# Performance work log

Measured on AMD Instinct MI355X. Metric: run time of the kernel, lower is better.

Reference implementation:

```python
import jax, jax.numpy as jnp
import numpy as np

B, LA, LB = 16, 2048, 2048
DA, DB, DH = 768, 512, 512
EPS = 1e-5


def _layer_norm(x, g, b):
    mu = jnp.mean(x, axis=-1, keepdims=True)
    var = jnp.var(x, axis=-1, keepdims=True)
    return (x - mu) * jax.lax.rsqrt(var + EPS) * g + b


def setup_inputs() -> dict:
    key = jax.random.key(0)
    ks = jax.random.split(key, 12)
    s = lambda d: 1.0 / np.sqrt(d)
    return {
        "z_a": jax.random.normal(ks[0], (B, LA, DA), jnp.float32),
        "z_b": jax.random.normal(ks[1], (B, LB, DB), jnp.float32),
        "Wa": jax.random.uniform(ks[2], (DA, DH), jnp.float32, -s(DA), s(DA)),
        "ba": jnp.zeros((DH,), jnp.float32),
        "Wb": jax.random.uniform(ks[3], (DB, DH), jnp.float32, -s(DB), s(DB)),
        "bb": jnp.zeros((DH,), jnp.float32),
        "W_co": jax.random.normal(ks[4], (DH, DH), jnp.float32),
        "Woa": jax.random.uniform(ks[5], (DH, DA), jnp.float32, -s(DH), s(DH)),
        "boa": jnp.zeros((DA,), jnp.float32),
        "Wob": jax.random.uniform(ks[6], (DH, DB), jnp.float32, -s(DH), s(DH)),
        "bob": jnp.zeros((DB,), jnp.float32),
        "ga": jnp.ones((DA,), jnp.float32),
        "beta_a": jnp.zeros((DA,), jnp.float32),
        "gb": jnp.ones((DB,), jnp.float32),
        "beta_b": jnp.zeros((DB,), jnp.float32),
    }


def reference(z_a, z_b, Wa, ba, Wb, bb, W_co, Woa, boa, Wob, bob, ga, beta_a, gb, beta_b):
    # projections to shared hidden space
    h_a = jnp.einsum('bld,dh->blh', z_a, Wa) + ba          # (B, LA, DH)
    h_b = jnp.einsum('bld,dh->blh', z_b, Wb) + bb          # (B, LB, DH)
    # bilinear tanh co-attention scores
    C = jnp.tanh(jnp.einsum('bih,hk,bjk->bij', h_a, W_co, h_b))  # (B, LA, LB)
    attn_a = jax.nn.softmax(C, axis=-1)                    # rows: over LB
    attn_b = jax.nn.softmax(C.transpose(0, 2, 1), axis=-1) # cols: over LA
    h_a_co = jnp.einsum('bij,bjh->bih', attn_a, h_b)       # (B, LA, DH)
    h_b_co = jnp.einsum('bji,bih->bjh', attn_b, h_a)       # (B, LB, DH)
    z_a_co = jnp.einsum('blh,hd->bld', h_a_co, Woa) + boa
    z_b_co = jnp.einsum('blh,hd->bld', h_b_co, Wob) + bob
    z_a_out = _layer_norm(z_a + z_a_co, ga, beta_a)
    z_b_out = _layer_norm(z_b + z_b_co, gb, beta_b)
    return (z_a_out, z_b_out)
```

## Files before the change

### kernel.cpp

```cpp
#include <hip/hip_runtime.h>
#include <stdint.h>

typedef short bf16x8 __attribute__((ext_vector_type(8)));
typedef float f32x4 __attribute__((ext_vector_type(4)));

#define BM 256
#define BN 128
#define BK 64
#define ABUF_U 16384
#define BUF_U  24576

#define AS1 __attribute__((address_space(1)))
#define AS3 __attribute__((address_space(3)))

__device__ __forceinline__ ushort f2bf(float x) {
    uint32_t u = __float_as_uint(x);
    u += 0x7FFFu + ((u >> 16) & 1u);
    return (ushort)(u >> 16);
}

__device__ __forceinline__ void gload16(const void* g, void* l) {
    __builtin_amdgcn_global_load_lds((const AS1 void*)g, (AS3 void*)l, 16, 0, 0);
}

template<int MODE, bool HAS_BIAS, bool WRITE_T>
__global__ __launch_bounds__(512)
void gemm_bt(const ushort* __restrict__ Aptr_, const ushort* __restrict__ Bptr_,
             void* __restrict__ Cptr_, ushort* __restrict__ CTptr_,
             const float* __restrict__ bias, const float* __restrict__ resid_,
             float* __restrict__ rsum_, float* __restrict__ csum_,
             const float* __restrict__ scale_,
             int M, int N, int K, int lda, int ldb, int ldc,
             long sA, long sB, long sC, long sCT, long sSum,
             int ldct, int rbshift)
{
    extern __shared__ ushort smem[];

    const int z    = blockIdx.z;
    const int m0   = blockIdx.x * BM;
    const int n0   = blockIdx.y * BN;
    const int tid  = threadIdx.x;
    const int lane = tid & 63;
    const int wave = tid >> 6;
    const int wr   = wave >> 2;
    const int wcn  = wave & 3;
    const int g    = lane >> 4, c = lane & 15;

    const ushort* Ap = Aptr_ + z * sA;
    const ushort* Bp = Bptr_ + z * sB;

    long aoff[4]; int aLds[4];
    #pragma unroll
    for (int u = 0; u < 4; ++u) {
        const int li  = u * 512 + tid;
        const int row = li >> 3;
        const int gck = (li & 7) ^ (row & 7);
        aoff[u] = (long)(m0 + row) * lda + gck * 8;
        aLds[u] = li * 8;
    }
    long boff[2]; int bLds[2];
    #pragma unroll
    for (int v = 0; v < 2; ++v) {
        const int li  = v * 512 + tid;
        const int row = li >> 3;
        const int gck = (li & 7) ^ (row & 7);
        boff[v] = (long)(n0 + row) * ldb + gck * 8;
        bLds[v] = li * 8;
    }

    auto stage3 = [&](int kt, ushort* As, ushort* Bs, int q) {
        if (q == 0) {
            gload16(Ap + aoff[0] + kt, As + aLds[0]);
            gload16(Ap + aoff[1] + kt, As + aLds[1]);
            gload16(Ap + aoff[2] + kt, As + aLds[2]);
        } else {
            gload16(Ap + aoff[3] + kt, As + aLds[3]);
            gload16(Bp + boff[0] + kt, Bs + bLds[0]);
            gload16(Bp + boff[1] + kt, Bs + bLds[1]);
        }
    };

    f32x4 acc[8][2] = {};

    const int nk = K / BK;
    stage3(0, smem, smem + ABUF_U, 0);
    stage3(0, smem, smem + ABUF_U, 1);
    stage3(BK, smem + BUF_U, smem + BUF_U + ABUF_U, 0);
    stage3(BK, smem + BUF_U, smem + BUF_U + ABUF_U, 1);
    asm volatile("s_waitcnt vmcnt(6)" ::: "memory");
    __builtin_amdgcn_s_barrier();

    int bt = 0;
    for (int t = 0; t < nk; ++t) {
        const int b2 = (bt + 2 >= 3) ? bt - 1 : bt + 2;
        ushort* As  = smem + bt * BUF_U;
        ushort* Bs  = As + ABUF_U;
        ushort* As2 = smem + b2 * BUF_U;
        ushort* Bs2 = As2 + ABUF_U;
        const bool pf = (t + 2 < nk);

        #pragma unroll
        for (int q = 0; q < 2; ++q) {
            bf16x8 af[8], bfr[2];
            #pragma unroll
            for (int mi = 0; mi < 8; ++mi) {
                const int row = wr * 128 + mi * 16 + c;
                const int ckq = (q * 4 + g) ^ (row & 7);
                af[mi] = *(const bf16x8*)&As[row * BK + ckq * 8];
            }
            #pragma unroll
            for (int ni = 0; ni < 2; ++ni) {
                const int row = wcn * 32 + ni * 16 + c;
                const int ckq = (q * 4 + g) ^ (row & 7);
                bfr[ni] = *(const bf16x8*)&Bs[row * BK + ckq * 8];
            }
            if (pf) stage3((t + 2) * BK, As2, Bs2, q);
            if (q == 1) {
                if (pf) asm volatile("s_waitcnt vmcnt(6)" ::: "memory");
                else    asm volatile("s_waitcnt vmcnt(0)" ::: "memory");
            }
            asm volatile("" ::: "memory");
            __builtin_amdgcn_s_barrier();
            __builtin_amdgcn_s_setprio(1);
            #pragma unroll
            for (int mi = 0; mi < 8; ++mi)
                #pragma unroll
                for (int ni = 0; ni < 2; ++ni)
                    acc[mi][ni] = __builtin_amdgcn_mfma_f32_16x16x32_bf16(af[mi], bfr[ni], acc[mi][ni], 0, 0, 0);
            __builtin_amdgcn_s_setprio(0);
            asm volatile("" ::: "memory");
            __builtin_amdgcn_s_barrier();
        }
        bt = (bt + 1 == 3) ? 0 : bt + 1;
    }

    if constexpr (MODE == 0) {
        ushort* Cp = (ushort*)Cptr_ + z * sC;
        #pragma unroll
        for (int mi = 0; mi < 8; ++mi) {
            const int row = m0 + wr * 128 + mi * 16 + g * 4;
            #pragma unroll
            for (int ni = 0; ni < 2; ++ni) {
                const int col = n0 + wcn * 32 + ni * 16 + c;
                const float bv = HAS_BIAS ? bias[col] : 0.f;
                ushort v[4];
                #pragma unroll
                for (int r = 0; r < 4; ++r) v[r] = f2bf(acc[mi][ni][r] + bv);
                #pragma unroll
                for (int r = 0; r < 4; ++r) Cp[(long)(row + r) * ldc + col] = v[r];
                if constexpr (WRITE_T) {
                    const int bb = row >> rbshift;
                    const int ii = row & ((1 << rbshift) - 1);
                    *(ushort4*)&CTptr_[(long)bb * sCT + (long)col * ldct + ii] =
                        make_ushort4(v[0], v[1], v[2], v[3]);
                }
            }
        }
    } else if constexpr (MODE == 1) {
        ushort* Ep  = (ushort*)Cptr_ + z * sC;
        ushort* ETp = CTptr_ + z * sCT;
        float* rs = rsum_ + z * sSum;
        float* cs = csum_ + z * sSum;
        float rowpart[8][4] = {};
        float colpart[2] = {};
        #pragma unroll
        for (int mi = 0; mi < 8; ++mi) {
            const int row = m0 + wr * 128 + mi * 16 + g * 4;
            #pragma unroll
            for (int ni = 0; ni < 2; ++ni) {
                const int col = n0 + wcn * 32 + ni * 16 + c;
                ushort v[4];
                #pragma unroll
                for (int r = 0; r < 4; ++r) {
                    const float s = acc[mi][ni][r];
                    const float t = 1.f - 2.f / (__expf(2.f * s) + 1.f);
                    const float e = __expf(t);
                    rowpart[mi][r] += e;
                    colpart[ni]    += e;
                    v[r] = f2bf(e);
                }
                #pragma unroll
                for (int r = 0; r < 4; ++r) Ep[(long)(row + r) * ldc + col] = v[r];
                *(ushort4*)&ETp[(long)col * ldct + row] = make_ushort4(v[0], v[1], v[2], v[3]);
            }
        }
        #pragma unroll
        for (int mi = 0; mi < 8; ++mi) {
            #pragma unroll
            for (int r = 0; r < 4; ++r) {
                float v = rowpart[mi][r];
                v += __shfl_xor(v, 1); v += __shfl_xor(v, 2);
                v += __shfl_xor(v, 4); v += __shfl_xor(v, 8);
                if (c == 0) atomicAdd(&rs[m0 + wr * 128 + mi * 16 + g * 4 + r], v);
            }
        }
        #pragma unroll
        for (int ni = 0; ni < 2; ++ni) {
            float v = colpart[ni];
            v += __shfl_xor(v, 16); v += __shfl_xor(v, 32);
            if (g == 0) atomicAdd(&cs[n0 + wcn * 32 + ni * 16 + c], v);
        }
    } else if constexpr (MODE == 2) {
        const float* sc = scale_ + z * sSum;
        ushort* Cp = (ushort*)Cptr_ + z * sC;
        #pragma unroll
        for (int mi = 0; mi < 8; ++mi) {
            const int row = m0 + wr * 128 + mi * 16 + g * 4;
            float rcp[4];
            #pragma unroll
            for (int r = 0; r < 4; ++r) rcp[r] = 1.f / sc[row + r];
            #pragma unroll
            for (int ni = 0; ni < 2; ++ni) {
                const int col = n0 + wcn * 32 + ni * 16 + c;
                #pragma unroll
                for (int r = 0; r < 4; ++r)
                    Cp[(long)(row + r) * ldc + col] = f2bf(acc[mi][ni][r] * rcp[r]);
            }
        }
    } else {
        float* Co = (float*)Cptr_;
        #pragma unroll
        for (int mi = 0; mi < 8; ++mi) {
            const int row = m0 + wr * 128 + mi * 16 + g * 4;
            #pragma unroll
            for (int ni = 0; ni < 2; ++ni) {
                const int col = n0 + wcn * 32 + ni * 16 + c;
                const float bv = bias[col];
                #pragma unroll
                for (int r = 0; r < 4; ++r) {
                    const long idx = (long)(row + r) * ldc + col;
                    Co[idx] = acc[mi][ni][r] + bv + resid_[idx];
                }
            }
        }
    }
}

__global__ __launch_bounds__(256)
void cast32to16(const float* __restrict__ in, ushort* __restrict__ out, long n) {
    const long stride = (long)gridDim.x * 256 * 8;
    for (long i = ((long)blockIdx.x * 256 + threadIdx.x) * 8; i < n; i += stride) {
        const float4 f0 = *(const float4*)(in + i);
        const float4 f1 = *(const float4*)(in + i + 4);
        uint4 w;
        w.x = (uint)f2bf(f0.x) | ((uint)f2bf(f0.y) << 16);
        w.y = (uint)f2bf(f0.z) | ((uint)f2bf(f0.w) << 16);
        w.z = (uint)f2bf(f1.x) | ((uint)f2bf(f1.y) << 16);
        w.w = (uint)f2bf(f1.z) | ((uint)f2bf(f1.w) << 16);
        *(uint4*)(out + i) = w;
    }
}

__global__ __launch_bounds__(256)
void tcast(const float* __restrict__ in, ushort* __restrict__ out, int R, int C) {
    __shared__ float t[32][33];
    const int bx = blockIdx.x * 32, by = blockIdx.y * 32;
    const int tx = threadIdx.x, ty = threadIdx.y;
    for (int i = ty; i < 32; i += 8) {
        const int r = by + i, cc = bx + tx;
        if (r < R && cc < C) t[i][tx] = in[(long)r * C + cc];
    }
    __syncthreads();
    for (int i = ty; i < 32; i += 8) {
        const int cc = bx + i, r = by + tx;
        if (cc < C && r < R) out[(long)cc * R + r] = f2bf(t[tx][i]);
    }
}

template<int D>
__global__ __launch_bounds__(256)
void ln_rows(float* __restrict__ y, const float* __restrict__ gam, const float* __restrict__ bet) {
    constexpr int NV = D / 256;
    const long row = blockIdx.x;
    float* p = y + row * D;
    const int tid = threadIdx.x;
    float v[NV];
    float s = 0.f, s2 = 0.f;
    #pragma unroll
    for (int k = 0; k < NV; ++k) {
        v[k] = p[tid + k * 256];
        s += v[k]; s2 += v[k] * v[k];
    }
    #pragma unroll
    for (int off = 1; off < 64; off <<= 1) {
        s  += __shfl_xor(s, off);
        s2 += __shfl_xor(s2, off);
    }
    __shared__ float ws[4], ws2[4];
    const int wave = tid >> 6, lane = tid & 63;
    if (lane == 0) { ws[wave] = s; ws2[wave] = s2; }
    __syncthreads();
    s  = ws[0] + ws[1] + ws[2] + ws[3];
    s2 = ws2[0] + ws2[1] + ws2[2] + ws2[3];
    const float mu  = s / D;
    const float var = s2 / D - mu * mu;
    const float rstd = rsqrtf(var + 1e-5f);
    #pragma unroll
    for (int k = 0; k < NV; ++k) {
        const int i = tid + k * 256;
        p[i] = (v[k] - mu) * rstd * gam[i] + bet[i];
    }
}

extern "C" void kernel_launch(void* const* d_in, const int* in_sizes, int n_in,
                              void* d_out, int out_size, void* d_ws, size_t ws_size,
                              hipStream_t stream)
{
    (void)in_sizes; (void)n_in; (void)out_size; (void)ws_size;
    const float* z_a    = (const float*)d_in[0];
    const float* z_b    = (const float*)d_in[1];
    const float* Wa     = (const float*)d_in[2];
    const float* ba     = (const float*)d_in[3];
    const float* Wb     = (const float*)d_in[4];
    const float* bb     = (const float*)d_in[5];
    const float* Wco    = (const float*)d_in[6];
    const float* Woa    = (const float*)d_in[7];
    const float* boa    = (const float*)d_in[8];
    const float* Wob    = (const float*)d_in[9];
    const float* bob    = (const float*)d_in[10];
    const float* ga     = (const float*)d_in[11];
    const float* beta_a = (const float*)d_in[12];
    const float* gb     = (const float*)d_in[13];
    const float* beta_b = (const float*)d_in[14];

    const int Bn = 16, LA = 2048, LB = 2048, DA = 768, DB = 512, DH = 512;
    const long MA = (long)Bn * LA;
    const long MB = (long)Bn * LB;

    char* w = (char*)d_ws;
    size_t off = 0;
    auto alc = [&](size_t bytes) { void* p = w + off; off += (bytes + 255) & ~(size_t)255; return p; };

    ushort* WaT  = (ushort*)alc((size_t)DH * DA * 2);
    ushort* WbT  = (ushort*)alc((size_t)DH * DB * 2);
    ushort* WcoT = (ushort*)alc((size_t)DH * DH * 2);
    ushort* WoaT = (ushort*)alc((size_t)DA * DH * 2);
    ushort* WobT = (ushort*)alc((size_t)DB * DH * 2);
    ushort* h_a  = (ushort*)alc((size_t)MA * DH * 2);
    ushort* h_b  = (ushort*)alc((size_t)MB * DH * 2);
    ushort* h_aT = (ushort*)alc((size_t)Bn * DH * LA * 2);
    ushort* h_bT = (ushort*)alc((size_t)Bn * DH * LB * 2);
    ushort* Ma   = (ushort*)alc((size_t)MA * DH * 2);
    ushort* E    = (ushort*)alc((size_t)Bn * LA * LB * 2);
    ushort* ET   = (ushort*)alc((size_t)Bn * LB * LA * 2);
    ushort* Pa   = (ushort*)alc((size_t)MA * DH * 2);
    ushort* Pb   = (ushort*)alc((size_t)MB * DH * 2);
    float*  rsum = (float*)alc((size_t)Bn * LA * 4);
    float*  csum = (float*)alc((size_t)Bn * LB * 4);

    ushort* za16 = E;
    ushort* zb16 = E + (size_t)MA * DA;

    dim3 blk(512, 1, 1);
    dim3 blk256(256, 1, 1);
    dim3 tb(32, 8, 1);
    const int SHM = 3 * BUF_U * 2;

    tcast<<<dim3(DH / 32, DA / 32, 1), tb, 0, stream>>>(Wa,  WaT,  DA, DH);
    tcast<<<dim3(DH / 32, DB / 32, 1), tb, 0, stream>>>(Wb,  WbT,  DB, DH);
    tcast<<<dim3(DH / 32, DH / 32, 1), tb, 0, stream>>>(Wco, WcoT, DH, DH);
    tcast<<<dim3(DA / 32, DH / 32, 1), tb, 0, stream>>>(Woa, WoaT, DH, DA);
    tcast<<<dim3(DB / 32, DH / 32, 1), tb, 0, stream>>>(Wob, WobT, DH, DB);

    cast32to16<<<dim3(2048, 1, 1), blk256, 0, stream>>>(z_a, za16, MA * DA);
    cast32to16<<<dim3(2048, 1, 1), blk256, 0, stream>>>(z_b, zb16, MB * DB);

    hipMemsetAsync(rsum, 0, (size_t)Bn * (LA + LB) * sizeof(float), stream);

    gemm_bt<0, true, true><<<dim3(MA / BM, DH / BN, 1), blk, SHM, stream>>>(
        za16, WaT, h_a, h_aT, ba, nullptr, nullptr, nullptr, nullptr,
        (int)MA, DH, DA, DA, DA, DH, 0, 0, 0, (long)DH * LA, 0, LA, 11);

    gemm_bt<0, true, true><<<dim3(MB / BM, DH / BN, 1), blk, SHM, stream>>>(
        zb16, WbT, h_b, h_bT, bb, nullptr, nullptr, nullptr, nullptr,
        (int)MB, DH, DB, DB, DB, DH, 0, 0, 0, (long)DH * LB, 0, LB, 11);

    gemm_bt<0, false, false><<<dim3(MA / BM, DH / BN, 1), blk, SHM, stream>>>(
        h_a, WcoT, Ma, nullptr, nullptr, nullptr, nullptr, nullptr, nullptr,
        (int)MA, DH, DH, DH, DH, DH, 0, 0, 0, 0, 0, 0, 0);

    gemm_bt<1, false, false><<<dim3(LA / BM, LB / BN, Bn), blk, SHM, stream>>>(
        Ma, h_b, E, ET, nullptr, nullptr, rsum, csum, nullptr,
        LA, LB, DH, DH, DH, LB,
        (long)LA * DH, (long)LB * DH, (long)LA * LB, (long)LB * LA, LA, LA, 0);

    gemm_bt<2, false, false><<<dim3(LA / BM, DH / BN, Bn), blk, SHM, stream>>>(
        E, h_bT, Pa, nullptr, nullptr, nullptr, nullptr, nullptr, rsum,
        LA, DH, LB, LB, LB, DH,
        (long)LA * LB, (long)DH * LB, (long)LA * DH, 0, LA, 0, 0);

    gemm_bt<2, false, false><<<dim3(LB / BM, DH / BN, Bn), blk, SHM, stream>>>(
        ET, h_aT, Pb, nullptr, nullptr, nullptr, nullptr, nullptr, csum,
        LB, DH, LA, LA, LA, DH,
        (long)LB * LA, (long)DH * LA, (long)LB * DH, 0, LB, 0, 0);

    float* outA = (float*)d_out;
    float* outB = outA + MA * DA;

    gemm_bt<3, true, false><<<dim3(MA / BM, DA / BN, 1), blk, SHM, stream>>>(
        Pa, WoaT, outA, nullptr, boa, z_a, nullptr, nullptr, nullptr,
        (int)MA, DA, DH, DH, DH, DA, 0, 0, 0, 0, 0, 0, 0);

    gemm_bt<3, true, false><<<dim3(MB / BM, DB / BN, 1), blk, SHM, stream>>>(
        Pb, WobT, outB, nullptr, bob, z_b, nullptr, nullptr, nullptr,
        (int)MB, DB, DH, DH, DH, DB, 0, 0, 0, 0, 0, 0, 0);

    ln_rows<768><<<dim3((unsigned)MA, 1, 1), blk256, 0, stream>>>(outA, ga, beta_a);
    ln_rows<512><<<dim3((unsigned)MB, 1, 1), blk256, 0, stream>>>(outB, gb, beta_b);
}
```

Measured before the change: 781.6 us.

## Widen GEMM tile to 256x256 with double-buffered, interleaved load/MFMA schedule

```diff
diff --git a/kernel.cpp b/kernel.cpp
--- a/kernel.cpp
+++ b/kernel.cpp
@@ -5,10 +5,10 @@
 typedef float f32x4 __attribute__((ext_vector_type(4)));
 
 #define BM 256
-#define BN 128
+#define BN 256
 #define BK 64
 #define ABUF_U 16384
-#define BUF_U  24576
+#define BUF_U  32768
 
 #define AS1 __attribute__((address_space(1)))
 #define AS3 __attribute__((address_space(3)))
@@ -23,8 +23,14 @@
     __builtin_amdgcn_global_load_lds((const AS1 void*)g, (AS3 void*)l, 16, 0, 0);
 }
 
+#define ISSUE2(kt, buf, i0)                                                          \
+    do {                                                                             \
+        gload16(((i0) < 4 ? Ap : Bp) + goff[i0] + (kt), smem + (buf)*BUF_U + loff[i0]); \
+        gload16((((i0)+1) < 4 ? Ap : Bp) + goff[(i0)+1] + (kt), smem + (buf)*BUF_U + loff[(i0)+1]); \
+    } while (0)
+
 template<int MODE, bool HAS_BIAS, bool WRITE_T>
-__global__ __launch_bounds__(512)
+__global__ __launch_bounds__(512, 2)
 void gemm_bt(const ushort* __restrict__ Aptr_, const ushort* __restrict__ Bptr_,
              void* __restrict__ Cptr_, ushort* __restrict__ CTptr_,
              const float* __restrict__ bias, const float* __restrict__ resid_,
@@ -49,89 +55,94 @@
     const ushort* Ap = Aptr_ + z * sA;
     const ushort* Bp = Bptr_ + z * sB;
 
-    long aoff[4]; int aLds[4];
+    long goff[8]; int loff[8];
     #pragma unroll
     for (int u = 0; u < 4; ++u) {
         const int li  = u * 512 + tid;
         const int row = li >> 3;
         const int gck = (li & 7) ^ (row & 7);
-        aoff[u] = (long)(m0 + row) * lda + gck * 8;
-        aLds[u] = li * 8;
-    }
-    long boff[2]; int bLds[2];
-    #pragma unroll
-    for (int v = 0; v < 2; ++v) {
-        const int li  = v * 512 + tid;
-        const int row = li >> 3;
-        const int gck = (li & 7) ^ (row & 7);
-        boff[v] = (long)(n0 + row) * ldb + gck * 8;
-        bLds[v] = li * 8;
-    }
-
-    auto stage3 = [&](int kt, ushort* As, ushort* Bs, int q) {
-        if (q == 0) {
-            gload16(Ap + aoff[0] + kt, As + aLds[0]);
-            gload16(Ap + aoff[1] + kt, As + aLds[1]);
-            gload16(Ap + aoff[2] + kt, As + aLds[2]);
+        goff[u]     = (long)(m0 + row) * lda + gck * 8;
+        loff[u]     = li * 8;
+        goff[u + 4] = (long)(n0 + row) * ldb + gck * 8;
+        loff[u + 4] = ABUF_U + li * 8;
+    }
+
+    f32x4 acc[8][4] = {};
+
+    const int nk = K / BK;
+    ISSUE2(0, 0, 0); ISSUE2(0, 0, 2); ISSUE2(0, 0, 4); ISSUE2(0, 0, 6);
+
+    for (int t = 0; t < nk; ++t) {
+        const int cur = t & 1, nxt = cur ^ 1;
+        const ushort* As = smem + cur * BUF_U;
+        const ushort* Bs = As + ABUF_U;
+        const bool pf = (t + 1 < nk);
+        const int kt1 = (t + 1) * BK;
+
+        if (pf) {
+            ISSUE2(kt1, nxt, 0);
+            asm volatile("s_waitcnt vmcnt(2)" ::: "memory");
         } else {
-            gload16(Ap + aoff[3] + kt, As + aLds[3]);
-            gload16(Bp + boff[0] + kt, Bs + bLds[0]);
-            gload16(Bp + boff[1] + kt, Bs + bLds[1]);
-        }
-    };
-
-    f32x4 acc[8][2] = {};
-
-    const int nk = K / BK;
-    stage3(0, smem, smem + ABUF_U, 0);
-    stage3(0, smem, smem + ABUF_U, 1);
-    stage3(BK, smem + BUF_U, smem + BUF_U + ABUF_U, 0);
-    stage3(BK, smem + BUF_U, smem + BUF_U + ABUF_U, 1);
-    asm volatile("s_waitcnt vmcnt(6)" ::: "memory");
-    __builtin_amdgcn_s_barrier();
-
-    int bt = 0;
-    for (int t = 0; t < nk; ++t) {
-        const int b2 = (bt + 2 >= 3) ? bt - 1 : bt + 2;
-        ushort* As  = smem + bt * BUF_U;
-        ushort* Bs  = As + ABUF_U;
-        ushort* As2 = smem + b2 * BUF_U;
-        ushort* Bs2 = As2 + ABUF_U;
-        const bool pf = (t + 2 < nk);
-
-        #pragma unroll
-        for (int q = 0; q < 2; ++q) {
-            bf16x8 af[8], bfr[2];
+            asm volatile("s_waitcnt vmcnt(0)" ::: "memory");
+        }
+        __builtin_amdgcn_s_barrier();
+
+        bf16x8 af[8], bfr2[2];
+
+        auto ldA = [&](int kk) {
             #pragma unroll
             for (int mi = 0; mi < 8; ++mi) {
                 const int row = wr * 128 + mi * 16 + c;
-                const int ckq = (q * 4 + g) ^ (row & 7);
+                const int ckq = (kk * 4 + g) ^ (row & 7);
                 af[mi] = *(const bf16x8*)&As[row * BK + ckq * 8];
             }
-            #pragma unroll
-            for (int ni = 0; ni < 2; ++ni) {
-                const int row = wcn * 32 + ni * 16 + c;
-                const int ckq = (q * 4 + g) ^ (row & 7);
-                bfr[ni] = *(const bf16x8*)&Bs[row * BK + ckq * 8];
-            }
-            if (pf) stage3((t + 2) * BK, As2, Bs2, q);
-            if (q == 1) {
-                if (pf) asm volatile("s_waitcnt vmcnt(6)" ::: "memory");
-                else    asm volatile("s_waitcnt vmcnt(0)" ::: "memory");
-            }
-            asm volatile("" ::: "memory");
-            __builtin_amdgcn_s_barrier();
+        };
+        auto ldB = [&](int kk, int nh) {
+            #pragma unroll
+            for (int u = 0; u < 2; ++u) {
+                const int row = wcn * 64 + (nh * 2 + u) * 16 + c;
+                const int ckq = (kk * 4 + g) ^ (row & 7);
+                bfr2[u] = *(const bf16x8*)&Bs[row * BK + ckq * 8];
+            }
+        };
+        auto mm = [&](int nh) {
             __builtin_amdgcn_s_setprio(1);
             #pragma unroll
             for (int mi = 0; mi < 8; ++mi)
                 #pragma unroll
-                for (int ni = 0; ni < 2; ++ni)
-                    acc[mi][ni] = __builtin_amdgcn_mfma_f32_16x16x32_bf16(af[mi], bfr[ni], acc[mi][ni], 0, 0, 0);
+                for (int u = 0; u < 2; ++u)
+                    acc[mi][nh * 2 + u] = __builtin_amdgcn_mfma_f32_16x16x32_bf16(
+                        af[mi], bfr2[u], acc[mi][nh * 2 + u], 0, 0, 0);
             __builtin_amdgcn_s_setprio(0);
-            asm volatile("" ::: "memory");
-            __builtin_amdgcn_s_barrier();
-        }
-        bt = (bt + 1 == 3) ? 0 : bt + 1;
+        };
+
+        ldA(0); ldB(0, 0);
+        if (pf) ISSUE2(kt1, nxt, 2);
+        __builtin_amdgcn_s_barrier();
+        asm volatile("s_waitcnt lgkmcnt(0)" ::: "memory");
+        __builtin_amdgcn_sched_barrier(0);
+        mm(0);
+        __builtin_amdgcn_s_barrier();
+        ldB(0, 1);
+        if (pf) ISSUE2(kt1, nxt, 4);
+        __builtin_amdgcn_s_barrier();
+        asm volatile("s_waitcnt lgkmcnt(0)" ::: "memory");
+        __builtin_amdgcn_sched_barrier(0);
+        mm(1);
+        __builtin_amdgcn_s_barrier();
+        ldA(1); ldB(1, 0);
+        if (pf) ISSUE2(kt1, nxt, 6);
+        __builtin_amdgcn_s_barrier();
+        asm volatile("s_waitcnt lgkmcnt(0)" ::: "memory");
+        __builtin_amdgcn_sched_barrier(0);
+        mm(0);
+        __builtin_amdgcn_s_barrier();
+        ldB(1, 1);
+        __builtin_amdgcn_s_barrier();
+        asm volatile("s_waitcnt lgkmcnt(0)" ::: "memory");
+        __builtin_amdgcn_sched_barrier(0);
+        mm(1);
+        __builtin_amdgcn_s_barrier();
     }
 
     if constexpr (MODE == 0) {
@@ -140,8 +151,8 @@
         for (int mi = 0; mi < 8; ++mi) {
             const int row = m0 + wr * 128 + mi * 16 + g * 4;
             #pragma unroll
-            for (int ni = 0; ni < 2; ++ni) {
-                const int col = n0 + wcn * 32 + ni * 16 + c;
+            for (int ni = 0; ni < 4; ++ni) {
+                const int col = n0 + wcn * 64 + ni * 16 + c;
                 const float bv = HAS_BIAS ? bias[col] : 0.f;
                 ushort v[4];
                 #pragma unroll
@@ -162,13 +173,13 @@
         float* rs = rsum_ + z * sSum;
         float* cs = csum_ + z * sSum;
         float rowpart[8][4] = {};
-        float colpart[2] = {};
+        float colpart[4] = {};
         #pragma unroll
         for (int mi = 0; mi < 8; ++mi) {
             const int row = m0 + wr * 128 + mi * 16 + g * 4;
             #pragma unroll
-            for (int ni = 0; ni < 2; ++ni) {
-                const int col = n0 + wcn * 32 + ni * 16 + c;
+            for (int ni = 0; ni < 4; ++ni) {
+                const int col = n0 + wcn * 64 + ni * 16 + c;
                 ushort v[4];
                 #pragma unroll
                 for (int r = 0; r < 4; ++r) {
@@ -195,10 +206,10 @@
             }
         }
         #pragma unroll
-        for (int ni = 0; ni < 2; ++ni) {
+        for (int ni = 0; ni < 4; ++ni) {
             float v = colpart[ni];
             v += __shfl_xor(v, 16); v += __shfl_xor(v, 32);
-            if (g == 0) atomicAdd(&cs[n0 + wcn * 32 + ni * 16 + c], v);
+            if (g == 0) atomicAdd(&cs[n0 + wcn * 64 + ni * 16 + c], v);
         }
     } else if constexpr (MODE == 2) {
         const float* sc = scale_ + z * sSum;
@@ -210,8 +221,8 @@
             #pragma unroll
             for (int r = 0; r < 4; ++r) rcp[r] = 1.f / sc[row + r];
             #pragma unroll
-            for (int ni = 0; ni < 2; ++ni) {
-                const int col = n0 + wcn * 32 + ni * 16 + c;
+            for (int ni = 0; ni < 4; ++ni) {
+                const int col = n0 + wcn * 64 + ni * 16 + c;
                 #pragma unroll
                 for (int r = 0; r < 4; ++r)
                     Cp[(long)(row + r) * ldc + col] = f2bf(acc[mi][ni][r] * rcp[r]);
@@ -223,8 +234,8 @@
         for (int mi = 0; mi < 8; ++mi) {
             const int row = m0 + wr * 128 + mi * 16 + g * 4;
             #pragma unroll
-            for (int ni = 0; ni < 2; ++ni) {
-                const int col = n0 + wcn * 32 + ni * 16 + c;
+            for (int ni = 0; ni < 4; ++ni) {
+                const int col = n0 + wcn * 64 + ni * 16 + c;
                 const float bv = bias[col];
                 #pragma unroll
                 for (int r = 0; r < 4; ++r) {
@@ -354,7 +365,7 @@
     dim3 blk(512, 1, 1);
     dim3 blk256(256, 1, 1);
     dim3 tb(32, 8, 1);
-    const int SHM = 3 * BUF_U * 2;
+    const int SHM = 2 * BUF_U * 2;
 
     tcast<<<dim3(DH / 32, DA / 32, 1), tb, 0, stream>>>(Wa,  WaT,  DA, DH);
     tcast<<<dim3(DH / 32, DB / 32, 1), tb, 0, stream>>>(Wb,  WbT,  DB, DH);
```

New measurement: 719.9 us. -7.9%, faster.
